# Kernel optimization log

Measured on AMD Instinct MI355X. Metric: run time of the kernel, lower is better.

Reference implementation:

```python
import jax, jax.numpy as jnp
import numpy as np

NUM_EMBEDDINGS = 8192
EMBEDDING_DIM = 256


def setup_inputs() -> dict:
    key = jax.random.key(0)
    kx, kw = jax.random.split(key)
    x = jax.random.normal(kx, (16384, EMBEDDING_DIM), dtype=jnp.float32)
    # nn.Embedding weight initialized uniform(-1/K, 1/K)
    bound = 1.0 / NUM_EMBEDDINGS
    weight = jax.random.uniform(kw, (NUM_EMBEDDINGS, EMBEDDING_DIM),
                                dtype=jnp.float32, minval=-bound, maxval=bound)
    return {"x": x, "weight": weight}


def reference(x, weight):
    # flatten to (N, D)
    flat_x = x.reshape(-1, EMBEDDING_DIM)
    distances = (jnp.sum(flat_x * flat_x, axis=1, keepdims=True)
                 + jnp.sum(weight * weight, axis=1)
                 - 2.0 * jnp.matmul(flat_x, weight.T))
    encoding_indices = jnp.argmin(distances, axis=1)  # (N,)
    quantized = weight[encoding_indices].reshape(x.shape)
    return quantized, encoding_indices
```

## Files before the change

kernel.cpp:

```cpp
#include <hip/hip_runtime.h>
#include <hip/hip_bf16.h>

#define NROWS 16384
#define NCODES 8192
#define DIM 256
#define BM 128
#define CPB 4096
#define CAP 24
#define MARGIN 3.0e-4f

typedef __attribute__((ext_vector_type(8))) short bf16x8;
typedef __attribute__((ext_vector_type(4))) float f32x4;

__device__ inline unsigned short f2bf(float f) {
    union { __hip_bfloat16 h; unsigned short u; } cv;
    cv.h = __float2bfloat16(f);
    return cv.u;
}
__device__ inline unsigned f2ord(float f) {
    unsigned u = __float_as_uint(f);
    return u ^ ((u >> 31) ? 0xFFFFFFFFu : 0x80000000u);
}
__device__ inline float ord2f(unsigned u) {
    unsigned v = (u & 0x80000000u) ? (u ^ 0x80000000u) : ~u;
    return __uint_as_float(v);
}

__device__ float pairwise256_sq(const float4* p) {
    float res[2];
    #pragma unroll
    for (int h = 0; h < 2; ++h) {
        float r[8];
        #pragma unroll
        for (int j = 0; j < 8; ++j) r[j] = 0.0f;
        #pragma unroll
        for (int g = 0; g < 16; ++g) {
            float4 v0 = p[h * 32 + g * 2];
            float4 v1 = p[h * 32 + g * 2 + 1];
            r[0] = __fadd_rn(r[0], __fmul_rn(v0.x, v0.x));
            r[1] = __fadd_rn(r[1], __fmul_rn(v0.y, v0.y));
            r[2] = __fadd_rn(r[2], __fmul_rn(v0.z, v0.z));
            r[3] = __fadd_rn(r[3], __fmul_rn(v0.w, v0.w));
            r[4] = __fadd_rn(r[4], __fmul_rn(v1.x, v1.x));
            r[5] = __fadd_rn(r[5], __fmul_rn(v1.y, v1.y));
            r[6] = __fadd_rn(r[6], __fmul_rn(v1.z, v1.z));
            r[7] = __fadd_rn(r[7], __fmul_rn(v1.w, v1.w));
        }
        res[h] = __fadd_rn(__fadd_rn(__fadd_rn(r[0], r[1]), __fadd_rn(r[2], r[3])),
                           __fadd_rn(__fadd_rn(r[4], r[5]), __fadd_rn(r[6], r[7])));
    }
    return __fadd_rn(res[0], res[1]);
}

__global__ __launch_bounds__(256) void sq_kernel(const float* __restrict__ x,
                                                 const float* __restrict__ w,
                                                 float* __restrict__ xsq,
                                                 float* __restrict__ wsq) {
    int gid = blockIdx.x * 256 + threadIdx.x;
    if (gid < NROWS)
        xsq[gid] = pairwise256_sq(reinterpret_cast<const float4*>(x + (size_t)gid * DIM));
    else
        wsq[gid - NROWS] =
            pairwise256_sq(reinterpret_cast<const float4*>(w + (size_t)(gid - NROWS) * DIM));
}

__global__ __launch_bounds__(256) void wfrag_kernel(const float* __restrict__ w,
                                                    unsigned short* __restrict__ whf) {
    int tid = blockIdx.x * 256 + threadIdx.x;
    int L = tid & 63;
    int rest = tid >> 6;
    int c16 = rest & 511;
    int k32 = rest >> 9;
    int code = c16 * 16 + (L & 15);
    int k = k32 * 32 + (L >> 4) * 8;
    const float4* p = reinterpret_cast<const float4*>(w + (size_t)code * DIM + k);
    float4 u0 = p[0], u1 = p[1];
    unsigned short tmp[8];
    tmp[0] = f2bf(u0.x); tmp[1] = f2bf(u0.y); tmp[2] = f2bf(u0.z); tmp[3] = f2bf(u0.w);
    tmp[4] = f2bf(u1.x); tmp[5] = f2bf(u1.y); tmp[6] = f2bf(u1.z); tmp[7] = f2bf(u1.w);
    *reinterpret_cast<uint4*>(whf + (size_t)tid * 8) = *reinterpret_cast<uint4*>(tmp);
}

__global__ __launch_bounds__(512, 2)
void vq_main(const float* __restrict__ x, const float* __restrict__ w,
             const unsigned short* __restrict__ whf,
             const float* __restrict__ wsq, const float* __restrict__ xsq,
             unsigned long long* __restrict__ best64g) {
    __shared__ unsigned short afrag[8 * 8 * 64 * 8];
    __shared__ unsigned rowmin[BM];
    __shared__ int cnt[BM];
    __shared__ int cand[BM][CAP];

    const int tid = threadIdx.x;
    const int lane = tid & 63;
    const int wv = tid >> 6;
    const int lm = lane & 15;
    const int lq = lane >> 4;

    const int blk = blockIdx.x;
    const int xcd = blk & 7;
    const int split = xcd & 1;
    const int rowGroup = (xcd >> 1) * 32 + (blk >> 3);
    const int rowBase = rowGroup * BM;
    const int codeBase = split * CPB;

    if (tid < BM) { rowmin[tid] = 0xFFFFFFFFu; cnt[tid] = 0; }

    {
        const int rg = wv;
        const float* xr = x + (size_t)(rowBase + rg * 16 + lm) * DIM + lq * 8;
        #pragma unroll
        for (int k32 = 0; k32 < 8; ++k32) {
            float4 u0 = *reinterpret_cast<const float4*>(xr + k32 * 32);
            float4 u1 = *reinterpret_cast<const float4*>(xr + k32 * 32 + 4);
            unsigned short t8[8];
            t8[0] = f2bf(u0.x); t8[1] = f2bf(u0.y); t8[2] = f2bf(u0.z); t8[3] = f2bf(u0.w);
            t8[4] = f2bf(u1.x); t8[5] = f2bf(u1.y); t8[6] = f2bf(u1.z); t8[7] = f2bf(u1.w);
            *reinterpret_cast<uint4*>(afrag + ((rg * 8 + k32) * 64 + lane) * 8) =
                *reinterpret_cast<uint4*>(t8);
        }
    }
    __syncthreads();

    const int waveCode16 = (codeBase + wv * 512) >> 4;

    for (int p = 0; p < 8; ++p) {
        const int pbase16 = waveCode16 + p * 4;
        f32x4 acc[8][4];
        #pragma unroll
        for (int rg = 0; rg < 8; ++rg)
            #pragma unroll
            for (int cf = 0; cf < 4; ++cf)
                acc[rg][cf] = (f32x4){0.f, 0.f, 0.f, 0.f};

        bf16x8 bb[2][4];
        #pragma unroll
        for (int cf = 0; cf < 4; ++cf)
            bb[0][cf] = *reinterpret_cast<const bf16x8*>(
                whf + (((size_t)(pbase16 + cf)) * 64 + lane) * 8);

        #pragma unroll
        for (int k32 = 0; k32 < 8; ++k32) {
            const int cur = k32 & 1;
            if (k32 < 7) {
                #pragma unroll
                for (int cf = 0; cf < 4; ++cf)
                    bb[cur ^ 1][cf] = *reinterpret_cast<const bf16x8*>(
                        whf + (((size_t)((k32 + 1) * 512 + pbase16 + cf)) * 64 + lane) * 8);
            }
            bf16x8 a[8];
            #pragma unroll
            for (int rg = 0; rg < 8; ++rg)
                a[rg] = *reinterpret_cast<const bf16x8*>(
                    afrag + ((rg * 8 + k32) * 64 + lane) * 8);
            #pragma unroll
            for (int cf = 0; cf < 4; ++cf)
                #pragma unroll
                for (int rg = 0; rg < 8; ++rg)
                    acc[rg][cf] = __builtin_amdgcn_mfma_f32_16x16x32_bf16(
                        a[rg], bb[cur][cf], acc[rg][cf], 0, 0, 0);
        }

        float wq[4];
        #pragma unroll
        for (int cf = 0; cf < 4; ++cf)
            wq[cf] = wsq[(pbase16 + cf) * 16 + lm];

        float mloc[32];
        #pragma unroll
        for (int rg = 0; rg < 8; ++rg) {
            #pragma unroll
            for (int r = 0; r < 4; ++r) {
                float m = __builtin_huge_valf();
                #pragma unroll
                for (int cf = 0; cf < 4; ++cf)
                    m = fminf(m, fmaf(-2.f, acc[rg][cf][r], wq[cf]));
                mloc[rg * 4 + r] = m;
                float rm = m;
                rm = fminf(rm, __shfl_xor(rm, 1, 64));
                rm = fminf(rm, __shfl_xor(rm, 2, 64));
                rm = fminf(rm, __shfl_xor(rm, 4, 64));
                rm = fminf(rm, __shfl_xor(rm, 8, 64));
                if (lm == 0)
                    atomicMin(&rowmin[rg * 16 + lq * 4 + r], f2ord(rm));
            }
        }
        #pragma unroll
        for (int rg = 0; rg < 8; ++rg) {
            #pragma unroll
            for (int r = 0; r < 4; ++r) {
                const int row = rg * 16 + lq * 4 + r;
                float limit = ord2f(rowmin[row]) + MARGIN;
                if (mloc[rg * 4 + r] <= limit) {
                    #pragma unroll
                    for (int cf = 0; cf < 4; ++cf) {
                        float s = fmaf(-2.f, acc[rg][cf][r], wq[cf]);
                        if (s <= limit) {
                            int pos = atomicAdd(&cnt[row], 1);
                            if (pos < CAP)
                                cand[row][pos] = (pbase16 + cf) * 16 + lm;
                        }
                    }
                }
            }
        }
    }
    __syncthreads();

    for (int slot = tid; slot < BM * CAP; slot += 512) {
        int row = slot / CAP, pos = slot - (slot / CAP) * CAP;
        int n = cnt[row] < CAP ? cnt[row] : CAP;
        if (pos < n) {
            int c = cand[row][pos];
            const float* xr = x + (size_t)(rowBase + row) * DIM;
            const float* wr = w + (size_t)c * DIM;
            float d = 0.f;
            for (int k = 0; k < DIM; k += 4) {
                float4 a = *reinterpret_cast<const float4*>(xr + k);
                float4 b = *reinterpret_cast<const float4*>(wr + k);
                d = fmaf(a.x, b.x, d);
                d = fmaf(a.y, b.y, d);
                d = fmaf(a.z, b.z, d);
                d = fmaf(a.w, b.w, d);
            }
            float t1 = __fadd_rn(xsq[rowBase + row], wsq[c]);
            float s = __fsub_rn(t1, __fadd_rn(d, d));
            unsigned long long key =
                ((unsigned long long)__float_as_uint(s) << 32) | (unsigned)c;
            atomicMin(best64g + rowBase + row, key);
        }
    }
}

__global__ __launch_bounds__(256)
void out_kernel(const float* __restrict__ w,
                const unsigned long long* __restrict__ best64g,
                float* __restrict__ out_q, float* __restrict__ out_idx) {
    int r = blockIdx.x * 4 + (threadIdx.x >> 6);
    int lane = threadIdx.x & 63;
    unsigned long long key = best64g[r];
    int idx = (int)(key & 0xFFFFFFFFu);
    float4 v = reinterpret_cast<const float4*>(w + (size_t)idx * DIM)[lane];
    reinterpret_cast<float4*>(out_q + (size_t)r * DIM)[lane] = v;
    if (lane == 0) out_idx[r] = (float)idx;
}

extern "C" void kernel_launch(void* const* d_in, const int* in_sizes, int n_in,
                              void* d_out, int out_size, void* d_ws, size_t ws_size,
                              hipStream_t stream) {
    const float* x = (const float*)d_in[0];
    const float* w = (const float*)d_in[1];
    float* out_q = (float*)d_out;
    float* out_idx = (float*)d_out + (size_t)NROWS * DIM;

    unsigned short* whf = (unsigned short*)d_ws;
    float* wsq = (float*)((char*)d_ws + (size_t)NCODES * DIM * 2);
    float* xsq = wsq + NCODES;
    unsigned long long* best64g = (unsigned long long*)(xsq + NROWS);

    wfrag_kernel<<<(NCODES * DIM / 8) / 256, 256, 0, stream>>>(w, whf);
    sq_kernel<<<(NROWS + NCODES) / 256, 256, 0, stream>>>(x, w, xsq, wsq);
    hipMemsetAsync(best64g, 0xFF, (size_t)NROWS * 8, stream);
    vq_main<<<256, 512, 0, stream>>>(x, w, whf, wsq, xsq, best64g);
    out_kernel<<<NROWS / 4, 256, 0, stream>>>(w, best64g, out_q, out_idx);
}
```

Measured before the change: 264.1 us.

## Split codebook 8 ways across blocks and fuse prep kernels with memset

The main kernel now splits the codebook into eight 1024-code slices per 128-row tile, launching 1024 blocks instead of 256, so each block does a quarter of the previous work and the GPU is filled more evenly. The B-fragment prefetch now carries across the two code passes to hide the first load. The weight fragment conversion, the squared norms and the best-index initialisation are merged into one prep kernel, replacing three launches. The cost is that each row tile of x is converted into shared memory eight times instead of twice, the candidate capacity drops to 16, and the XCD-aware block mapping is removed.

```diff
diff --git a/kernel.cpp b/kernel.cpp
--- a/kernel.cpp
+++ b/kernel.cpp
@@ -5,8 +5,8 @@
 #define NCODES 8192
 #define DIM 256
 #define BM 128
-#define CPB 4096
-#define CAP 24
+#define CPB 1024
+#define CAP 16
 #define MARGIN 3.0e-4f
 
 typedef __attribute__((ext_vector_type(8))) short bf16x8;
@@ -52,33 +52,35 @@
     return __fadd_rn(res[0], res[1]);
 }
 
-__global__ __launch_bounds__(256) void sq_kernel(const float* __restrict__ x,
-                                                 const float* __restrict__ w,
-                                                 float* __restrict__ xsq,
-                                                 float* __restrict__ wsq) {
+#define WFRAG_UNITS (NCODES * DIM / 8)
+__global__ __launch_bounds__(256)
+void prep_kernel(const float* __restrict__ x, const float* __restrict__ w,
+                 unsigned short* __restrict__ whf, float* __restrict__ xsq,
+                 float* __restrict__ wsq, unsigned long long* __restrict__ best64g) {
     int gid = blockIdx.x * 256 + threadIdx.x;
-    if (gid < NROWS)
-        xsq[gid] = pairwise256_sq(reinterpret_cast<const float4*>(x + (size_t)gid * DIM));
-    else
-        wsq[gid - NROWS] =
-            pairwise256_sq(reinterpret_cast<const float4*>(w + (size_t)(gid - NROWS) * DIM));
-}
-
-__global__ __launch_bounds__(256) void wfrag_kernel(const float* __restrict__ w,
-                                                    unsigned short* __restrict__ whf) {
-    int tid = blockIdx.x * 256 + threadIdx.x;
-    int L = tid & 63;
-    int rest = tid >> 6;
-    int c16 = rest & 511;
-    int k32 = rest >> 9;
-    int code = c16 * 16 + (L & 15);
-    int k = k32 * 32 + (L >> 4) * 8;
-    const float4* p = reinterpret_cast<const float4*>(w + (size_t)code * DIM + k);
-    float4 u0 = p[0], u1 = p[1];
-    unsigned short tmp[8];
-    tmp[0] = f2bf(u0.x); tmp[1] = f2bf(u0.y); tmp[2] = f2bf(u0.z); tmp[3] = f2bf(u0.w);
-    tmp[4] = f2bf(u1.x); tmp[5] = f2bf(u1.y); tmp[6] = f2bf(u1.z); tmp[7] = f2bf(u1.w);
-    *reinterpret_cast<uint4*>(whf + (size_t)tid * 8) = *reinterpret_cast<uint4*>(tmp);
+    if (gid < WFRAG_UNITS) {
+        int L = gid & 63;
+        int rest = gid >> 6;
+        int c16 = rest & 511;
+        int k32 = rest >> 9;
+        int code = c16 * 16 + (L & 15);
+        int k = k32 * 32 + (L >> 4) * 8;
+        const float4* p = reinterpret_cast<const float4*>(w + (size_t)code * DIM + k);
+        float4 u0 = p[0], u1 = p[1];
+        unsigned short tmp[8];
+        tmp[0] = f2bf(u0.x); tmp[1] = f2bf(u0.y); tmp[2] = f2bf(u0.z); tmp[3] = f2bf(u0.w);
+        tmp[4] = f2bf(u1.x); tmp[5] = f2bf(u1.y); tmp[6] = f2bf(u1.z); tmp[7] = f2bf(u1.w);
+        *reinterpret_cast<uint4*>(whf + (size_t)gid * 8) = *reinterpret_cast<uint4*>(tmp);
+    } else {
+        int t = gid - WFRAG_UNITS;
+        if (t < NROWS) {
+            xsq[t] = pairwise256_sq(reinterpret_cast<const float4*>(x + (size_t)t * DIM));
+            best64g[t] = ~0ull;
+        } else if (t < NROWS + NCODES) {
+            int c = t - NROWS;
+            wsq[c] = pairwise256_sq(reinterpret_cast<const float4*>(w + (size_t)c * DIM));
+        }
+    }
 }
 
 __global__ __launch_bounds__(512, 2)
@@ -98,11 +100,9 @@
     const int lq = lane >> 4;
 
     const int blk = blockIdx.x;
-    const int xcd = blk & 7;
-    const int split = xcd & 1;
-    const int rowGroup = (xcd >> 1) * 32 + (blk >> 3);
-    const int rowBase = rowGroup * BM;
-    const int codeBase = split * CPB;
+    const int split = blk & 7;
+    const int rowBase = (blk >> 3) * BM;
+    const int wave16 = split * 64 + wv * 8;
 
     if (tid < BM) { rowmin[tid] = 0xFFFFFFFFu; cnt[tid] = 0; }
 
@@ -122,22 +122,21 @@
     }
     __syncthreads();
 
-    const int waveCode16 = (codeBase + wv * 512) >> 4;
-
-    for (int p = 0; p < 8; ++p) {
-        const int pbase16 = waveCode16 + p * 4;
+    bf16x8 bb[2][4];
+    #pragma unroll
+    for (int cf = 0; cf < 4; ++cf)
+        bb[0][cf] = *reinterpret_cast<const bf16x8*>(
+            whf + (((size_t)(wave16 + cf)) * 64 + lane) * 8);
+
+    #pragma unroll
+    for (int p = 0; p < 2; ++p) {
+        const int pbase16 = wave16 + p * 4;
         f32x4 acc[8][4];
         #pragma unroll
         for (int rg = 0; rg < 8; ++rg)
             #pragma unroll
             for (int cf = 0; cf < 4; ++cf)
                 acc[rg][cf] = (f32x4){0.f, 0.f, 0.f, 0.f};
-
-        bf16x8 bb[2][4];
-        #pragma unroll
-        for (int cf = 0; cf < 4; ++cf)
-            bb[0][cf] = *reinterpret_cast<const bf16x8*>(
-                whf + (((size_t)(pbase16 + cf)) * 64 + lane) * 8);
 
         #pragma unroll
         for (int k32 = 0; k32 < 8; ++k32) {
@@ -147,6 +146,11 @@
                 for (int cf = 0; cf < 4; ++cf)
                     bb[cur ^ 1][cf] = *reinterpret_cast<const bf16x8*>(
                         whf + (((size_t)((k32 + 1) * 512 + pbase16 + cf)) * 64 + lane) * 8);
+            } else if (p == 0) {
+                #pragma unroll
+                for (int cf = 0; cf < 4; ++cf)
+                    bb[cur ^ 1][cf] = *reinterpret_cast<const bf16x8*>(
+                        whf + (((size_t)(pbase16 + 4 + cf)) * 64 + lane) * 8);
             }
             bf16x8 a[8];
             #pragma unroll
@@ -258,9 +262,8 @@
     float* xsq = wsq + NCODES;
     unsigned long long* best64g = (unsigned long long*)(xsq + NROWS);
 
-    wfrag_kernel<<<(NCODES * DIM / 8) / 256, 256, 0, stream>>>(w, whf);
-    sq_kernel<<<(NROWS + NCODES) / 256, 256, 0, stream>>>(x, w, xsq, wsq);
-    hipMemsetAsync(best64g, 0xFF, (size_t)NROWS * 8, stream);
-    vq_main<<<256, 512, 0, stream>>>(x, w, whf, wsq, xsq, best64g);
+    prep_kernel<<<(WFRAG_UNITS + NROWS + NCODES) / 256, 256, 0, stream>>>(
+        x, w, whf, xsq, wsq, best64g);
+    vq_main<<<(NROWS / BM) * 8, 512, 0, stream>>>(x, w, whf, wsq, xsq, best64g);
     out_kernel<<<NROWS / 4, 256, 0, stream>>>(w, best64g, out_q, out_idx);
 }
```

Result: slower. 380.3 us (+44.0%).
